# Optimization experiments

Measured on AMD Instinct MI355X. Metric: run time of the kernel, lower is better.

Reference implementation:

```python
import jax, jax.numpy as jnp
import numpy as np

N, M, E, H = 4096, 16384, 512, 8
D = E // H  # head dim = 64


def _rms(x, g, eps=1e-6):
    return x * jax.lax.rsqrt(jnp.mean(jnp.square(x), axis=-1, keepdims=True) + eps) * g


def _split(x):
    # (rows, E) -> (rows, H, D)
    return x.reshape(x.shape[0], H, D)


def _sdpa(q, k, v):
    # Faithful to the source layout: SDPA on (rows, H, D) tensors, i.e. per-row
    # attention over the H heads (tiny HxH softmax per node).
    s = jnp.einsum('nhd,ngd->nhg', q, k) / jnp.sqrt(jnp.asarray(D, q.dtype))
    a = jax.nn.softmax(s, axis=-1)
    return jnp.einsum('nhg,ngd->nhd', a, v).reshape(-1, E)


def setup_inputs() -> dict:
    key = jax.random.key(0)
    ks = jax.random.split(key, 25)
    w = lambda k, s, sc: jax.random.normal(k, s, dtype=jnp.float32) * sc
    se = 1.0 / np.sqrt(E)   # Linear(E, E) init scale
    sm = 1.0 / np.sqrt(M)   # Linear(M, N) init scale
    inp = {
        'x_node': jax.random.normal(ks[0], (N, E), dtype=jnp.float32),
        'x_edge': jax.random.normal(ks[1], (M, E), dtype=jnp.float32),
        # sparse-ish binary adjacency, avg degree ~8
        'adj': (jax.random.uniform(ks[2], (N, N)) < 0.002).astype(jnp.float32),
        # per-branch QKV weights (4 separate MultiHeadAttention modules)
        'Wq_hh': w(ks[3], (E, E), se), 'Wk_hh': w(ks[4], (E, E), se), 'Wv_hh': w(ks[5], (E, E), se),
        'Wq_ee': w(ks[6], (E, E), se), 'Wk_ee': w(ks[7], (E, E), se), 'Wv_ee': w(ks[8], (E, E), se),
        'Wq_he': w(ks[9], (E, E), se), 'Wk_he': w(ks[10], (E, E), se), 'Wv_he': w(ks[11], (E, E), se),
        'Wq_eh': w(ks[12], (E, E), se), 'Wk_eh': w(ks[13], (E, E), se), 'Wv_eh': w(ks[14], (E, E), se),
        # shape_proj (edges -> nodes) weights, one per module that uses it
        'Wp1_he': w(ks[15], (N, M), sm),
        'Wp1_eh': w(ks[16], (N, M), sm),
        'Wp1_ee': w(ks[17], (N, M), sm),
        # RMSNorm gains
        'g_n': jnp.ones((E,), jnp.float32),
        'g_e': jnp.ones((E,), jnp.float32),
        'g2': jnp.ones((E,), jnp.float32),
        # FeedForward
        'Wf1': w(ks[18], (E, 4 * E), se), 'bf1': jnp.zeros((4 * E,), jnp.float32),
        'Wf2': w(ks[19], (4 * E, E), 1.0 / np.sqrt(4 * E)), 'bf2': jnp.zeros((E,), jnp.float32),
    }
    return inp


def reference(x_node, x_edge, adj,
              Wq_hh, Wk_hh, Wv_hh, Wq_ee, Wk_ee, Wv_ee,
              Wq_he, Wk_he, Wv_he, Wq_eh, Wk_eh, Wv_eh,
              Wp1_he, Wp1_eh, Wp1_ee,
              g_n, g_e, g2, Wf1, bf1, Wf2, bf2):
    h = _rms(x_node, g_n)   # (N, E)
    e = _rms(x_edge, g_e)   # (M, E)

    # hh: adjacency injected into the node query branch
    q = jnp.einsum('nm,mhd->nhd', adj, _split(h @ Wq_hh))
    out_hh = _sdpa(q, _split(h @ Wk_hh), _split(h @ Wv_hh))

    # ee: edge queries/keys projected to node rows via shape_proj
    q = jnp.einsum('nm,mhd->nhd', Wp1_ee, _split(e @ Wq_ee))
    k = jnp.einsum('nm,mhd->nhd', Wp1_ee, _split(e @ Wk_ee))
    out_ee = _sdpa(q, k, _split(h @ Wv_ee))

    # eh: edge query projected to node rows, node key
    q = jnp.einsum('nm,mhd->nhd', Wp1_eh, _split(e @ Wq_eh))
    out_eh = _sdpa(q, _split(h @ Wk_eh), _split(h @ Wv_eh))

    # he: node query, edge key projected to node rows
    k = jnp.einsum('nm,mhd->nhd', Wp1_he, _split(e @ Wk_he))
    out_he = _sdpa(_split(h @ Wq_he), k, _split(h @ Wv_he))

    x = out_hh + out_ee + out_eh + out_he          # (N, E)
    y = _rms(x, g2)
    return jax.nn.gelu(y @ Wf1 + bf1, approximate=False) @ Wf2 + bf2
```

## Files before the change

kernel.cpp:

```cpp
#include <hip/hip_runtime.h>
#include <cstdint>


typedef unsigned short u16;
typedef __bf16 bf16x8 __attribute__((ext_vector_type(8)));
typedef float f32x4 __attribute__((ext_vector_type(4)));

__device__ __forceinline__ u16 f2bf(float f) {
    unsigned u = __float_as_uint(f);
    return (u16)((u + 0x7fffu + ((u >> 16) & 1u)) >> 16);
}
__device__ __forceinline__ float bf2f(u16 u) { return __uint_as_float(((unsigned)u) << 16); }
__device__ __forceinline__ float gelu_exact(float x) {
    return 0.5f * x * (1.0f + erff(x * 0.70710678118654752f));
}

__device__ __forceinline__ void gload_lds16(const void* g, void* l) {
    __builtin_amdgcn_global_load_lds(
        (const __attribute__((address_space(1))) unsigned int*)(uintptr_t)g,
        (__attribute__((address_space(3))) unsigned int*)(unsigned int)(uintptr_t)l,
        16, 0, 0);
}

#define SCHED0 __builtin_amdgcn_sched_barrier(0)

__device__ __forceinline__ void swz_block(int& bx, int& by, int& bz) {
    const int nx = gridDim.x, ny = gridDim.y;
    const int nwg = nx * ny * gridDim.z;
    int lin = blockIdx.x + nx * (blockIdx.y + ny * blockIdx.z);
    const int chunk = nwg >> 3;
    lin = (lin & 7) * chunk + (lin >> 3);
    bx = lin % nx;
    lin /= nx;
    by = lin % ny;
    bz = lin / ny;
}

template <bool SWZ>
__global__ __launch_bounds__(256) void cvt_f32_bf16(const float* __restrict__ in,
                                                    u16* __restrict__ out, size_t n8) {
    size_t i = (size_t)blockIdx.x * 256 + threadIdx.x;
    size_t stride = (size_t)gridDim.x * 256;
    for (; i < n8; i += stride) {
        float4 a = ((const float4*)in)[i * 2];
        float4 b = ((const float4*)in)[i * 2 + 1];
        u16 r[8] = {f2bf(a.x), f2bf(a.y), f2bf(a.z), f2bf(a.w),
                    f2bf(b.x), f2bf(b.y), f2bf(b.z), f2bf(b.w)};
        size_t o = i;
        if constexpr (SWZ) o = (i & ~(size_t)63) | ((i & 63) ^ ((i >> 7) & 3));
        ((uint4*)out)[o] = *(const uint4*)r;
    }
}

__global__ __launch_bounds__(256) void transpose_cvt(const float* __restrict__ in,
                                                     u16* __restrict__ out, int R, int C) {
    __shared__ float tile[32][33];
    int c0 = blockIdx.x * 32, r0 = blockIdx.y * 32;
    int tx = threadIdx.x & 31, ty = threadIdx.x >> 5;
#pragma unroll
    for (int i = 0; i < 4; ++i)
        tile[ty + i * 8][tx] = in[(size_t)(r0 + ty + i * 8) * C + c0 + tx];
    __syncthreads();
#pragma unroll
    for (int i = 0; i < 4; ++i) {
        int orow = c0 + ty + i * 8;
        out[(size_t)orow * R + ((r0 + tx) ^ (((orow >> 1) & 3) << 3))] = f2bf(tile[tx][ty + i * 8]);
    }
}

struct W12 { const float* in[12]; u16* out[12]; };
__global__ __launch_bounds__(256) void transpose_cvt12(W12 w) {
    __shared__ float tile[32][33];
    const float* in = w.in[blockIdx.z];
    u16* out = w.out[blockIdx.z];
    int c0 = blockIdx.x * 32, r0 = blockIdx.y * 32;
    int tx = threadIdx.x & 31, ty = threadIdx.x >> 5;
#pragma unroll
    for (int i = 0; i < 4; ++i)
        tile[ty + i * 8][tx] = in[(size_t)(r0 + ty + i * 8) * 512 + c0 + tx];
    __syncthreads();
#pragma unroll
    for (int i = 0; i < 4; ++i) {
        int orow = c0 + ty + i * 8;
        out[(size_t)orow * 512 + ((r0 + tx) ^ (((orow >> 1) & 3) << 3))] = f2bf(tile[tx][ty + i * 8]);
    }
}

__global__ __launch_bounds__(256) void transpose_u16(const u16* __restrict__ in,
                                                     u16* __restrict__ out, int R, int C) {
    __shared__ u16 tile[32][34];
    int c0 = blockIdx.x * 32, r0 = blockIdx.y * 32;
    int tx = threadIdx.x & 31, ty = threadIdx.x >> 5;
#pragma unroll
    for (int i = 0; i < 4; ++i)
        tile[ty + i * 8][tx] = in[(size_t)(r0 + ty + i * 8) * C + c0 + tx];
    __syncthreads();
#pragma unroll
    for (int i = 0; i < 4; ++i) {
        int orow = c0 + ty + i * 8;
        out[(size_t)orow * R + ((r0 + tx) ^ (((orow >> 1) & 3) << 3))] = tile[tx][ty + i * 8];
    }
}

template <bool SWZ>
__global__ __launch_bounds__(256) void rmsnorm_bf16(const float* __restrict__ x,
                                                    const float* __restrict__ g,
                                                    u16* __restrict__ out) {
    int row = blockIdx.x, tid = threadIdx.x;
    const float* xr = x + (size_t)row * 512;
    float2 v = *(const float2*)(xr + tid * 2);
    float ss = v.x * v.x + v.y * v.y;
#pragma unroll
    for (int o = 32; o; o >>= 1) ss += __shfl_down(ss, o);
    __shared__ float red[4];
    if ((tid & 63) == 0) red[tid >> 6] = ss;
    __syncthreads();
    float tot = red[0] + red[1] + red[2] + red[3];
    float rs = rsqrtf(tot * (1.0f / 512.0f) + 1e-6f);
    unsigned pack = (unsigned)f2bf(v.x * rs * g[tid * 2]) |
                    ((unsigned)f2bf(v.y * rs * g[tid * 2 + 1]) << 16);
    int o32 = SWZ ? (tid ^ (((row >> 1) & 3) << 2)) : tid;
    ((unsigned*)out)[(size_t)row * 256 + o32] = pack;
}

__global__ __launch_bounds__(256) void adj_spmm(const float* __restrict__ adj,
                                                const u16* __restrict__ h,
                                                u16* __restrict__ out) {
    const int wave = threadIdx.x >> 6, lane = threadIdx.x & 63;
    const int n = blockIdx.x * 4 + wave;
    const float* arow = adj + (size_t)n * 4096;
    float acc[8] = {0.f, 0.f, 0.f, 0.f, 0.f, 0.f, 0.f, 0.f};
    for (int j = 0; j < 64; ++j) {
        float v = arow[j * 64 + lane];
        unsigned long long mask = __ballot(v != 0.0f);
        while (mask) {
            int bit = __ffsll((long long)mask) - 1;
            mask &= mask - 1;
            int m = j * 64 + bit;
            float w = __shfl(v, bit);
            int cs = (lane & ~3) | ((lane & 3) ^ ((m >> 1) & 3));
            uint4 q = *(const uint4*)(h + (size_t)m * 512 + cs * 8);
            const u16* qu = (const u16*)&q;
#pragma unroll
            for (int t = 0; t < 8; ++t) acc[t] += w * bf2f(qu[t]);
        }
    }
    int co = (lane & ~3) | ((lane & 3) ^ ((n >> 1) & 3));
    u16 r[8];
#pragma unroll
    for (int t = 0; t < 8; ++t) r[t] = f2bf(acc[t]);
    *(uint4*)(out + (size_t)n * 512 + co * 8) = *(const uint4*)r;
}

template <int MODE>
__device__ __forceinline__ void gemm_tile_body(const u16* __restrict__ A,
                                               const u16* __restrict__ Bt,
                                               int N, int K, int k_begin, int k_end,
                                               int rowStart, int colStart,
                                               void* __restrict__ C,
                                               const float* __restrict__ bias) {
    __shared__ u16 Asm[128 * 32];
    __shared__ u16 Bsm[128 * 32];
    const int tid = threadIdx.x;
    const int wave = tid >> 6, lane = tid & 63;
    const int wr = wave >> 1, wc = wave & 1;

    f32x4 acc[4][4];
#pragma unroll
    for (int m = 0; m < 4; ++m)
#pragma unroll
        for (int n = 0; n < 4; ++n) acc[m][n] = f32x4{0.f, 0.f, 0.f, 0.f};

    const int off0 = (wave * 2 + 0) * 1024 + lane * 16;
    const int off1 = (wave * 2 + 1) * 1024 + lane * 16;
    const int r0 = off0 >> 6, k0e = (off0 & 63) >> 1;
    const int r1 = off1 >> 6, k1e = (off1 & 63) >> 1;
    const size_t Arow0 = (size_t)(rowStart + r0) * K + k0e;
    const size_t Arow1 = (size_t)(rowStart + r1) * K + k1e;
    const size_t Brow0 = (size_t)(colStart + r0) * K + k0e;
    const size_t Brow1 = (size_t)(colStart + r1) * K + k1e;
    u16* As0 = &Asm[(wave * 2 + 0) * 512];
    u16* As1 = &Asm[(wave * 2 + 1) * 512];
    u16* Bs0 = &Bsm[(wave * 2 + 0) * 512];
    u16* Bs1 = &Bsm[(wave * 2 + 1) * 512];

    const int rsel = lane & 15, ksel = lane >> 4;
    const int fsw = (ksel ^ ((rsel >> 1) & 3)) << 3;

    for (int kk = k_begin; kk < k_end; kk += 32) {
        gload_lds16(A + Arow0 + kk, As0);
        gload_lds16(A + Arow1 + kk, As1);
        gload_lds16(Bt + Brow0 + kk, Bs0);
        gload_lds16(Bt + Brow1 + kk, Bs1);
        __syncthreads();
        bf16x8 aF[4], bF[4];
#pragma unroll
        for (int m = 0; m < 4; ++m)
            aF[m] = *(const bf16x8*)&Asm[(wr * 64 + m * 16 + rsel) * 32 + fsw];
#pragma unroll
        for (int n = 0; n < 4; ++n)
            bF[n] = *(const bf16x8*)&Bsm[(wc * 64 + n * 16 + rsel) * 32 + fsw];
#pragma unroll
        for (int m = 0; m < 4; ++m)
#pragma unroll
            for (int n = 0; n < 4; ++n)
                acc[m][n] = __builtin_amdgcn_mfma_f32_16x16x32_bf16(aF[m], bF[n], acc[m][n], 0, 0, 0);
        __syncthreads();
    }

    const int cq = (lane >> 4) * 4, cr = lane & 15;
#pragma unroll
    for (int m = 0; m < 4; ++m) {
#pragma unroll
        for (int n = 0; n < 4; ++n) {
            int col = colStart + wc * 64 + n * 16 + cr;
#pragma unroll
            for (int j = 0; j < 4; ++j) {
                int row = rowStart + wr * 64 + m * 16 + cq + j;
                float v = acc[m][n][j];
                if constexpr (MODE == 0) {
                    ((u16*)C)[(size_t)row * N + col] = f2bf(v);
                } else if constexpr (MODE == 1) {
                    v = gelu_exact(v + bias[col]);
                    ((u16*)C)[(size_t)row * N + (col ^ (((row >> 1) & 3) << 3))] = f2bf(v);
                } else {
                    if (bias) v += bias[col];
                    atomicAdd(&((float*)C)[(size_t)row * N + col], v);
                }
            }
        }
    }
}

template <int MODE>
__global__ __launch_bounds__(256) void gemm_bt(const u16* __restrict__ A,
                                               const u16* __restrict__ Bt,
                                               void* __restrict__ C,
                                               const float* __restrict__ bias,
                                               int N, int K, int kLen) {
    int bx, by, bz;
    swz_block(bx, by, bz);
    const float* bb = (MODE == 3) ? ((bz == 0) ? bias : nullptr) : bias;
    int kb = bz * kLen;
    gemm_tile_body<MODE>(A, Bt, N, K, kb, kb + kLen, by * 128, bx * 128, C, bb);
}

struct Small12 { const u16* A[12]; const u16* W[12]; u16* C[12]; };
__global__ __launch_bounds__(256) void gemm_small12(Small12 s) {
    int bx, by, bz;
    swz_block(bx, by, bz);
    gemm_tile_body<0>(s.A[bz], s.W[bz], 512, 512, 0, 512, by * 128, bx * 128, s.C[bz], nullptr);
}

struct Big3 { const float* A[3]; };
__global__ __launch_bounds__(256, 2) void gemm_f32a(Big3 ba, const u16* __restrict__ Bt,
                                                    float* __restrict__ C0, int K) {
    __shared__ float Afs[3][4096];
    __shared__ u16 Bsm[3][4096];
    const int i = blockIdx.x;
    const int x = i & 7, j = i >> 3;
    const int bx = j & 3;
    const int g = x * 48 + (j >> 2);
    const int by = g & 31, bz = g >> 5;
    const int mat = bz >> 2, ks = bz & 3;
    const float* __restrict__ A = ba.A[mat];
    float* __restrict__ C = C0 + (size_t)mat * (4096 * 512);
    const int rowStart = by * 128, colStart = bx * 128;
    const int kLen = 4096;
    const int k0 = ks * kLen;

    const int tid = threadIdx.x;
    const int wave = tid >> 6, lane = tid & 63;
    const int wr = wave >> 1, wc = wave & 1;

    f32x4 acc[4][4];
#pragma unroll
    for (int mm = 0; mm < 4; ++mm)
#pragma unroll
        for (int n = 0; n < 4; ++n) acc[mm][n] = f32x4{0.f, 0.f, 0.f, 0.f};

    const int lrow = lane >> 3;
    const int slot = (lane & 7) ^ lrow;
    size_t asrc[4];
    int adst[4];
#pragma unroll
    for (int ii = 0; ii < 4; ++ii) {
        int row = wave * 32 + ii * 8 + lrow;
        asrc[ii] = (size_t)(rowStart + row) * K + slot * 4;
        adst[ii] = (wave * 4 + ii) * 256 + lane * 4;
    }

    const int off0 = (wave * 2 + 0) * 1024 + lane * 16;
    const int off1 = (wave * 2 + 1) * 1024 + lane * 16;
    const int br0 = off0 >> 6, bk0 = (off0 & 63) >> 1;
    const int br1 = off1 >> 6, bk1 = (off1 & 63) >> 1;
    const u16* Bp0 = Bt + (size_t)(colStart + br0) * K + bk0;
    const u16* Bp1 = Bt + (size_t)(colStart + br1) * K + bk1;
    const int ws0 = (wave * 2 + 0) * 512, ws1 = (wave * 2 + 1) * 512;

    const int rsel = lane & 15, ksel = lane >> 4;
    const int fsw = (ksel ^ ((rsel >> 1) & 3)) << 3;

    auto STAGE = [&](int buf, int kk) {
#pragma unroll
        for (int ii = 0; ii < 4; ++ii)
            gload_lds16(A + asrc[ii] + kk, &Afs[buf][adst[ii]]);
        gload_lds16(Bp0 + kk, &Bsm[buf][ws0]);
        gload_lds16(Bp1 + kk, &Bsm[buf][ws1]);
    };
    auto COMPUTE = [&](int buf) {
        bf16x8 aF[4], bF[4];
#pragma unroll
        for (int mm = 0; mm < 4; ++mm) {
            int R = wr * 64 + mm * 16 + rsel;
            const char* rb = (const char*)&Afs[buf][0] + R * 128;
            f32x4 lo = *(const f32x4*)(rb + ((((ksel << 1) | 0) ^ (R & 7)) << 4));
            f32x4 hi = *(const f32x4*)(rb + ((((ksel << 1) | 1) ^ (R & 7)) << 4));
            aF[mm][0] = (__bf16)lo[0]; aF[mm][1] = (__bf16)lo[1];
            aF[mm][2] = (__bf16)lo[2]; aF[mm][3] = (__bf16)lo[3];
            aF[mm][4] = (__bf16)hi[0]; aF[mm][5] = (__bf16)hi[1];
            aF[mm][6] = (__bf16)hi[2]; aF[mm][7] = (__bf16)hi[3];
        }
#pragma unroll
        for (int n = 0; n < 4; ++n)
            bF[n] = *(const bf16x8*)&Bsm[buf][(wc * 64 + n * 16 + rsel) * 32 + fsw];
#pragma unroll
        for (int mm = 0; mm < 4; ++mm)
#pragma unroll
            for (int n = 0; n < 4; ++n)
                acc[mm][n] = __builtin_amdgcn_mfma_f32_16x16x32_bf16(aF[mm], bF[n], acc[mm][n], 0, 0, 0);
    };
    auto STEP = [&](int sbuf, int cbuf, int kk) {
        STAGE(sbuf, kk);
        SCHED0;
        asm volatile("s_waitcnt vmcnt(12)");
        SCHED0;
        __builtin_amdgcn_s_barrier();
        SCHED0;
        COMPUTE(cbuf);
        SCHED0;
        __builtin_amdgcn_s_barrier();
        SCHED0;
    };

    STAGE(0, k0);
    STAGE(1, k0 + 32);
    SCHED0;

    int kk = k0 + 64;
    for (int it = 0; it < 42; ++it) {
        STEP(2, 0, kk);
        STEP(0, 1, kk + 32);
        STEP(1, 2, kk + 64);
        kk += 96;
    }
    asm volatile("s_waitcnt vmcnt(6)");
    SCHED0;
    __builtin_amdgcn_s_barrier();
    SCHED0;
    COMPUTE(0);
    SCHED0;
    __builtin_amdgcn_s_barrier();
    SCHED0;
    asm volatile("s_waitcnt vmcnt(0)");
    SCHED0;
    __builtin_amdgcn_s_barrier();
    SCHED0;
    COMPUTE(1);

    const int cq = (lane >> 4) * 4, cr = lane & 15;
#pragma unroll
    for (int mm = 0; mm < 4; ++mm)
#pragma unroll
        for (int n = 0; n < 4; ++n) {
            int col = colStart + wc * 64 + n * 16 + cr;
#pragma unroll
            for (int jj = 0; jj < 4; ++jj) {
                int row = rowStart + wr * 64 + mm * 16 + cq + jj;
                atomicAdd(&C[(size_t)row * 512 + col], acc[mm][n][jj]);
            }
        }
}

struct SP12 { const u16* p[12]; };
__global__ __launch_bounds__(256) void sdpa_fused(SP12 sp, const float* __restrict__ g2,
                                                  u16* __restrict__ y) {
    __shared__ float qb[4][8][65], kb[4][8][65], vb[4][8][65];
    __shared__ float aw[4][64];
    __shared__ float red[4];
    const int n = blockIdx.x, tid = threadIdx.x;
    const size_t base = (size_t)n * 512;
    const int e0 = tid * 2, hs = e0 >> 6, ds = e0 & 63;

#pragma unroll
    for (int br = 0; br < 4; ++br) {
        unsigned u;
        u = *(const unsigned*)(sp.p[br * 3 + 0] + base + e0);
        qb[br][hs][ds] = bf2f(u & 0xffffu); qb[br][hs][ds + 1] = bf2f(u >> 16);
        u = *(const unsigned*)(sp.p[br * 3 + 1] + base + e0);
        kb[br][hs][ds] = bf2f(u & 0xffffu); kb[br][hs][ds + 1] = bf2f(u >> 16);
        u = *(const unsigned*)(sp.p[br * 3 + 2] + base + e0);
        vb[br][hs][ds] = bf2f(u & 0xffffu); vb[br][hs][ds + 1] = bf2f(u >> 16);
    }
    __syncthreads();

    const int b = tid >> 6, h = (tid >> 3) & 7, g = tid & 7;
    float s = 0.f;
    const float* qr = &qb[b][h][0];
    const float* kr = &kb[b][g][0];
#pragma unroll
    for (int j = 0; j < 64; ++j) s += qr[j] * kr[j];
    s *= 0.125f;
    float mx = s;
#pragma unroll
    for (int o = 1; o < 8; o <<= 1) mx = fmaxf(mx, __shfl_xor(mx, o));
    float p = expf(s - mx);
    float sm = p;
#pragma unroll
    for (int o = 1; o < 8; o <<= 1) sm += __shfl_xor(sm, o);
    aw[b][(h << 3) | g] = p / sm;
    __syncthreads();

    float o0 = 0.f, o1 = 0.f;
#pragma unroll
    for (int bb = 0; bb < 4; ++bb)
#pragma unroll
        for (int gg = 0; gg < 8; ++gg) {
            float a = aw[bb][(hs << 3) | gg];
            o0 += a * vb[bb][gg][ds];
            o1 += a * vb[bb][gg][ds + 1];
        }

    float ss = o0 * o0 + o1 * o1;
#pragma unroll
    for (int o = 32; o; o >>= 1) ss += __shfl_down(ss, o);
    if ((tid & 63) == 0) red[tid >> 6] = ss;
    __syncthreads();
    float tot = red[0] + red[1] + red[2] + red[3];
    float rs = rsqrtf(tot * (1.0f / 512.0f) + 1e-6f);
    unsigned pack = (unsigned)f2bf(o0 * rs * g2[e0]) | ((unsigned)f2bf(o1 * rs * g2[e0 + 1]) << 16);
    ((unsigned*)y)[(size_t)n * 256 + (tid ^ (((n >> 1) & 3) << 2))] = pack;
}

extern "C" void kernel_launch(void* const* d_in, const int* in_sizes, int n_in,
                              void* d_out, int out_size, void* d_ws, size_t ws_size,
                              hipStream_t stream) {
    (void)in_sizes; (void)n_in; (void)out_size; (void)ws_size;
    const int N = 4096, M = 16384, E = 512;

    const float* x_node = (const float*)d_in[0];
    const float* x_edge = (const float*)d_in[1];
    const float* adj    = (const float*)d_in[2];
    const float* Wp1_he = (const float*)d_in[15];
    const float* Wp1_eh = (const float*)d_in[16];
    const float* Wp1_ee = (const float*)d_in[17];
    const float* g_n = (const float*)d_in[18];
    const float* g_e = (const float*)d_in[19];
    const float* g2  = (const float*)d_in[20];
    const float* Wf1 = (const float*)d_in[21];
    const float* bf1 = (const float*)d_in[22];
    const float* Wf2 = (const float*)d_in[23];
    const float* bf2 = (const float*)d_in[24];

    char* p = (char*)d_ws;
    auto alloc = [&](size_t b) { char* r = p; p += (b + 255) & ~(size_t)255; return r; };
    const size_t NP = (size_t)N * E;
    const size_t WSZ = (size_t)E * E;
    u16* h    = (u16*)alloc(NP * 2);
    u16* e    = (u16*)alloc((size_t)M * E * 2);
    u16* eT   = (u16*)alloc((size_t)M * E * 2);
    u16* Wt   = (u16*)alloc(12 * WSZ * 2);
    u16* Wf1T = (u16*)alloc((size_t)2048 * 512 * 2);
    u16* Wf2T = (u16*)alloc((size_t)512 * 2048 * 2);
    float* F3 = (float*)alloc(3 * NP * 4);
    u16* P3b  = (u16*)alloc(3 * NP * 2);
    u16* Ahb  = (u16*)alloc(NP * 2);
    u16* S12  = (u16*)alloc(12 * NP * 2);
    u16* y    = (u16*)alloc(NP * 2);
    u16* t    = (u16*)alloc((size_t)N * 2048 * 2);

    W12 w12;
    for (int i = 0; i < 12; ++i) { w12.in[i] = (const float*)d_in[3 + i]; w12.out[i] = Wt + i * WSZ; }
    transpose_cvt12<<<dim3(16, 16, 12), 256, 0, stream>>>(w12);
    transpose_cvt<<<dim3(64, 16), 256, 0, stream>>>(Wf1, Wf1T, 512, 2048);
    transpose_cvt<<<dim3(16, 64), 256, 0, stream>>>(Wf2, Wf2T, 2048, 512);

    rmsnorm_bf16<true><<<N, 256, 0, stream>>>(x_node, g_n, h);
    rmsnorm_bf16<false><<<M, 256, 0, stream>>>(x_edge, g_e, e);
    transpose_u16<<<dim3(16, 512), 256, 0, stream>>>(e, eT, M, 512);
    adj_spmm<<<1024, 256, 0, stream>>>(adj, h, Ahb);

    hipMemsetAsync(F3, 0, 3 * NP * 4, stream);
    Big3 bp; bp.A[0] = Wp1_ee; bp.A[1] = Wp1_eh; bp.A[2] = Wp1_he;
    gemm_f32a<<<dim3(1536), 256, 0, stream>>>(bp, eT, F3, M);
    cvt_f32_bf16<true><<<2048, 256, 0, stream>>>(F3, P3b, 3 * NP / 8);
    const u16* Peeb = P3b + 0 * NP;
    const u16* Pehb = P3b + 1 * NP;
    const u16* Pheb = P3b + 2 * NP;

    Small12 sb;
    const u16* aList[12] = {Ahb, h, h, Peeb, Peeb, h, Pehb, h, h, h, Pheb, h};
    const int wList[12]  = {0, 1, 2, 3, 4, 5, 9, 10, 11, 6, 7, 8};
    for (int i = 0; i < 12; ++i) {
        sb.A[i] = aList[i];
        sb.W[i] = Wt + wList[i] * WSZ;
        sb.C[i] = S12 + i * NP;
    }
    gemm_small12<<<dim3(4, 32, 12), 256, 0, stream>>>(sb);

    SP12 sp;
    for (int i = 0; i < 12; ++i) sp.p[i] = S12 + i * NP;
    sdpa_fused<<<N, 256, 0, stream>>>(sp, g2, y);

    gemm_bt<1><<<dim3(16, 32, 1), 256, 0, stream>>>(y, Wf1T, t, bf1, 2048, 512, 512);
    hipMemsetAsync(d_out, 0, NP * 4, stream);
    gemm_bt<3><<<dim3(4, 32, 2), 256, 0, stream>>>(t, Wf2T, d_out, bf2, 512, 2048, 1024);
}
```

Before: 630.4 us.

## Widen f32-A projection GEMM tile to full 512 columns with 8-way split-K

The big shape_proj GEMM (Wp1 f32 x eT bf16) now uses 512-thread blocks that each cover 128 rows by all 512 output columns, with split-K raised from 4 to 8 and the k-loop switched from triple- to double-buffered LDS. Each f32 A tile is read from global memory once instead of four times across column blocks, which cuts the dominant A traffic. In exchange there are twice as many atomicAdd partial sums into C, a larger B tile in LDS, twice the accumulator registers per wave, and a shallower prefetch pipeline that may expose load latency.

```diff
diff --git a/kernel.cpp b/kernel.cpp
--- a/kernel.cpp
+++ b/kernel.cpp
@@ -253,63 +253,63 @@
 }
 
 struct Big3 { const float* A[3]; };
-__global__ __launch_bounds__(256, 2) void gemm_f32a(Big3 ba, const u16* __restrict__ Bt,
+__global__ __launch_bounds__(512, 2) void gemm_f32a(Big3 ba, const u16* __restrict__ Bt,
                                                     float* __restrict__ C0, int K) {
-    __shared__ float Afs[3][4096];
-    __shared__ u16 Bsm[3][4096];
-    const int i = blockIdx.x;
-    const int x = i & 7, j = i >> 3;
-    const int bx = j & 3;
-    const int g = x * 48 + (j >> 2);
-    const int by = g & 31, bz = g >> 5;
-    const int mat = bz >> 2, ks = bz & 3;
+    __shared__ float Afs[2][4096];
+    __shared__ u16 Bsm[2][16384];
+    const int id = blockIdx.x;
+    const int by = id & 31, g = id >> 5;
+    const int ks = g & 7, mat = g >> 3;
     const float* __restrict__ A = ba.A[mat];
     float* __restrict__ C = C0 + (size_t)mat * (4096 * 512);
-    const int rowStart = by * 128, colStart = bx * 128;
-    const int kLen = 4096;
+    const int rowStart = by * 128;
+    const int kLen = 2048;
     const int k0 = ks * kLen;
+    const int nt = kLen >> 5;
 
     const int tid = threadIdx.x;
     const int wave = tid >> 6, lane = tid & 63;
-    const int wr = wave >> 1, wc = wave & 1;
-
-    f32x4 acc[4][4];
+    const int wr = wave >> 2, wq = wave & 3;
+
+    f32x4 acc[4][8];
 #pragma unroll
     for (int mm = 0; mm < 4; ++mm)
 #pragma unroll
-        for (int n = 0; n < 4; ++n) acc[mm][n] = f32x4{0.f, 0.f, 0.f, 0.f};
+        for (int n = 0; n < 8; ++n) acc[mm][n] = f32x4{0.f, 0.f, 0.f, 0.f};
 
     const int lrow = lane >> 3;
     const int slot = (lane & 7) ^ lrow;
-    size_t asrc[4];
-    int adst[4];
+    size_t asrc[2];
+    int adst[2];
+#pragma unroll
+    for (int ii = 0; ii < 2; ++ii) {
+        int s = wave * 2 + ii;
+        asrc[ii] = (size_t)(rowStart + s * 8 + lrow) * K + slot * 4;
+        adst[ii] = s * 256 + lane * 4;
+    }
+
+    size_t bsrc[4];
+    int bdst[4];
 #pragma unroll
     for (int ii = 0; ii < 4; ++ii) {
-        int row = wave * 32 + ii * 8 + lrow;
-        asrc[ii] = (size_t)(rowStart + row) * K + slot * 4;
-        adst[ii] = (wave * 4 + ii) * 256 + lane * 4;
-    }
-
-    const int off0 = (wave * 2 + 0) * 1024 + lane * 16;
-    const int off1 = (wave * 2 + 1) * 1024 + lane * 16;
-    const int br0 = off0 >> 6, bk0 = (off0 & 63) >> 1;
-    const int br1 = off1 >> 6, bk1 = (off1 & 63) >> 1;
-    const u16* Bp0 = Bt + (size_t)(colStart + br0) * K + bk0;
-    const u16* Bp1 = Bt + (size_t)(colStart + br1) * K + bk1;
-    const int ws0 = (wave * 2 + 0) * 512, ws1 = (wave * 2 + 1) * 512;
+        int s = wave * 4 + ii;
+        bsrc[ii] = (size_t)(s * 16 + (lane >> 2)) * K + (lane & 3) * 8;
+        bdst[ii] = s * 512 + lane * 8;
+    }
 
     const int rsel = lane & 15, ksel = lane >> 4;
     const int fsw = (ksel ^ ((rsel >> 1) & 3)) << 3;
 
     auto STAGE = [&](int buf, int kk) {
 #pragma unroll
+        for (int ii = 0; ii < 2; ++ii)
+            gload_lds16(A + asrc[ii] + kk, &Afs[buf][adst[ii]]);
+#pragma unroll
         for (int ii = 0; ii < 4; ++ii)
-            gload_lds16(A + asrc[ii] + kk, &Afs[buf][adst[ii]]);
-        gload_lds16(Bp0 + kk, &Bsm[buf][ws0]);
-        gload_lds16(Bp1 + kk, &Bsm[buf][ws1]);
+            gload_lds16(Bt + bsrc[ii] + kk, &Bsm[buf][bdst[ii]]);
     };
     auto COMPUTE = [&](int buf) {
-        bf16x8 aF[4], bF[4];
+        bf16x8 aF[4], bF[8];
 #pragma unroll
         for (int mm = 0; mm < 4; ++mm) {
             int R = wr * 64 + mm * 16 + rsel;
@@ -322,58 +322,47 @@
             aF[mm][6] = (__bf16)hi[2]; aF[mm][7] = (__bf16)hi[3];
         }
 #pragma unroll
-        for (int n = 0; n < 4; ++n)
-            bF[n] = *(const bf16x8*)&Bsm[buf][(wc * 64 + n * 16 + rsel) * 32 + fsw];
+        for (int n = 0; n < 8; ++n)
+            bF[n] = *(const bf16x8*)&Bsm[buf][(wq * 128 + n * 16 + rsel) * 32 + fsw];
 #pragma unroll
         for (int mm = 0; mm < 4; ++mm)
 #pragma unroll
-            for (int n = 0; n < 4; ++n)
+            for (int n = 0; n < 8; ++n)
                 acc[mm][n] = __builtin_amdgcn_mfma_f32_16x16x32_bf16(aF[mm], bF[n], acc[mm][n], 0, 0, 0);
     };
-    auto STEP = [&](int sbuf, int cbuf, int kk) {
-        STAGE(sbuf, kk);
-        SCHED0;
-        asm volatile("s_waitcnt vmcnt(12)");
-        SCHED0;
-        __builtin_amdgcn_s_barrier();
-        SCHED0;
-        COMPUTE(cbuf);
-        SCHED0;
-        __builtin_amdgcn_s_barrier();
-        SCHED0;
-    };
 
     STAGE(0, k0);
-    STAGE(1, k0 + 32);
-    SCHED0;
-
-    int kk = k0 + 64;
-    for (int it = 0; it < 42; ++it) {
-        STEP(2, 0, kk);
-        STEP(0, 1, kk + 32);
-        STEP(1, 2, kk + 64);
-        kk += 96;
-    }
-    asm volatile("s_waitcnt vmcnt(6)");
-    SCHED0;
-    __builtin_amdgcn_s_barrier();
-    SCHED0;
-    COMPUTE(0);
-    SCHED0;
-    __builtin_amdgcn_s_barrier();
-    SCHED0;
     asm volatile("s_waitcnt vmcnt(0)");
     SCHED0;
     __builtin_amdgcn_s_barrier();
     SCHED0;
-    COMPUTE(1);
+
+    int cur = 0;
+    for (int t = 0; t < nt - 1; ++t) {
+        STAGE(cur ^ 1, k0 + (t + 1) * 32);
+        SCHED0;
+        asm volatile("s_waitcnt vmcnt(6)");
+        SCHED0;
+        __builtin_amdgcn_s_barrier();
+        SCHED0;
+        COMPUTE(cur);
+        SCHED0;
+        __builtin_amdgcn_s_barrier();
+        SCHED0;
+        cur ^= 1;
+    }
+    asm volatile("s_waitcnt vmcnt(0)");
+    SCHED0;
+    __builtin_amdgcn_s_barrier();
+    SCHED0;
+    COMPUTE(cur);
 
     const int cq = (lane >> 4) * 4, cr = lane & 15;
 #pragma unroll
     for (int mm = 0; mm < 4; ++mm)
 #pragma unroll
-        for (int n = 0; n < 4; ++n) {
-            int col = colStart + wc * 64 + n * 16 + cr;
+        for (int n = 0; n < 8; ++n) {
+            int col = wq * 128 + n * 16 + cr;
 #pragma unroll
             for (int jj = 0; jj < 4; ++jj) {
                 int row = rowStart + wr * 64 + mm * 16 + cq + jj;
@@ -492,7 +481,7 @@
 
     hipMemsetAsync(F3, 0, 3 * NP * 4, stream);
     Big3 bp; bp.A[0] = Wp1_ee; bp.A[1] = Wp1_eh; bp.A[2] = Wp1_he;
-    gemm_f32a<<<dim3(1536), 256, 0, stream>>>(bp, eT, F3, M);
+    gemm_f32a<<<dim3(768), 512, 0, stream>>>(bp, eT, F3, M);
     cvt_f32_bf16<true><<<2048, 256, 0, stream>>>(F3, P3b, 3 * NP / 8);
     const u16* Peeb = P3b + 0 * NP;
     const u16* Pehb = P3b + 1 * NP;
```

After: 681.0 us. 8.0% more time.

## Load fp32 A operand directly to registers in shape-proj GEMM, cut LDS

Applied to the files above, without the earlier changes.

The fp32 Wp1 operand of the big edge-to-node GEMM is now read straight from global memory into registers, double-buffered in registers, and converted to bf16 there instead of being staged through LDS. Only the bf16 B tile stays in LDS, double-buffered instead of triple. Each wave now owns 32 rows by all 128 columns, and the launch uses the shared swizzle helper with occupancy raised to 3 blocks. This lowers LDS footprint and LDS read traffic, at the cost of uncoalesced-ish per-lane global loads for A and more B fragment reads per wave.

```diff
diff --git a/kernel.cpp b/kernel.cpp
--- a/kernel.cpp
+++ b/kernel.cpp
@@ -253,42 +253,30 @@
 }
 
 struct Big3 { const float* A[3]; };
-__global__ __launch_bounds__(256, 2) void gemm_f32a(Big3 ba, const u16* __restrict__ Bt,
-                                                    float* __restrict__ C0, int K) {
-    __shared__ float Afs[3][4096];
-    __shared__ u16 Bsm[3][4096];
-    const int i = blockIdx.x;
-    const int x = i & 7, j = i >> 3;
-    const int bx = j & 3;
-    const int g = x * 48 + (j >> 2);
-    const int by = g & 31, bz = g >> 5;
-    const int mat = bz >> 2, ks = bz & 3;
+__global__ __launch_bounds__(256, 3) void gemm_f32a(Big3 ba, const u16* __restrict__ Bt,
+                                                    float* __restrict__ C0, int K,
+                                                    int zPerMat, int kLen) {
+    __shared__ u16 Bsm[2][4096];
+    int bx, by, bz;
+    swz_block(bx, by, bz);
+    const int mat = bz / zPerMat, ks = bz - mat * zPerMat;
     const float* __restrict__ A = ba.A[mat];
     float* __restrict__ C = C0 + (size_t)mat * (4096 * 512);
     const int rowStart = by * 128, colStart = bx * 128;
-    const int kLen = 4096;
     const int k0 = ks * kLen;
 
     const int tid = threadIdx.x;
     const int wave = tid >> 6, lane = tid & 63;
-    const int wr = wave >> 1, wc = wave & 1;
-
-    f32x4 acc[4][4];
-#pragma unroll
-    for (int mm = 0; mm < 4; ++mm)
-#pragma unroll
-        for (int n = 0; n < 4; ++n) acc[mm][n] = f32x4{0.f, 0.f, 0.f, 0.f};
-
-    const int lrow = lane >> 3;
-    const int slot = (lane & 7) ^ lrow;
-    size_t asrc[4];
-    int adst[4];
-#pragma unroll
-    for (int ii = 0; ii < 4; ++ii) {
-        int row = wave * 32 + ii * 8 + lrow;
-        asrc[ii] = (size_t)(rowStart + row) * K + slot * 4;
-        adst[ii] = (wave * 4 + ii) * 256 + lane * 4;
-    }
+    const int rsel = lane & 15, ksel = lane >> 4;
+
+    f32x4 acc[2][8];
+#pragma unroll
+    for (int mm = 0; mm < 2; ++mm)
+#pragma unroll
+        for (int n = 0; n < 8; ++n) acc[mm][n] = f32x4{0.f, 0.f, 0.f, 0.f};
+
+    const float* Ap0 = A + (size_t)(rowStart + wave * 32 + 0 * 16 + rsel) * K + ksel * 8;
+    const float* Ap1 = A + (size_t)(rowStart + wave * 32 + 1 * 16 + rsel) * K + ksel * 8;
 
     const int off0 = (wave * 2 + 0) * 1024 + lane * 16;
     const int off1 = (wave * 2 + 1) * 1024 + lane * 16;
@@ -298,67 +286,82 @@
     const u16* Bp1 = Bt + (size_t)(colStart + br1) * K + bk1;
     const int ws0 = (wave * 2 + 0) * 512, ws1 = (wave * 2 + 1) * 512;
 
-    const int rsel = lane & 15, ksel = lane >> 4;
     const int fsw = (ksel ^ ((rsel >> 1) & 3)) << 3;
 
-    auto STAGE = [&](int buf, int kk) {
-#pragma unroll
-        for (int ii = 0; ii < 4; ++ii)
-            gload_lds16(A + asrc[ii] + kk, &Afs[buf][adst[ii]]);
+    auto STAGEB = [&](int buf, int kk) {
         gload_lds16(Bp0 + kk, &Bsm[buf][ws0]);
         gload_lds16(Bp1 + kk, &Bsm[buf][ws1]);
     };
-    auto COMPUTE = [&](int buf) {
-        bf16x8 aF[4], bF[4];
-#pragma unroll
-        for (int mm = 0; mm < 4; ++mm) {
-            int R = wr * 64 + mm * 16 + rsel;
-            const char* rb = (const char*)&Afs[buf][0] + R * 128;
-            f32x4 lo = *(const f32x4*)(rb + ((((ksel << 1) | 0) ^ (R & 7)) << 4));
-            f32x4 hi = *(const f32x4*)(rb + ((((ksel << 1) | 1) ^ (R & 7)) << 4));
-            aF[mm][0] = (__bf16)lo[0]; aF[mm][1] = (__bf16)lo[1];
-            aF[mm][2] = (__bf16)lo[2]; aF[mm][3] = (__bf16)lo[3];
-            aF[mm][4] = (__bf16)hi[0]; aF[mm][5] = (__bf16)hi[1];
-            aF[mm][6] = (__bf16)hi[2]; aF[mm][7] = (__bf16)hi[3];
-        }
-#pragma unroll
-        for (int n = 0; n < 4; ++n)
-            bF[n] = *(const bf16x8*)&Bsm[buf][(wc * 64 + n * 16 + rsel) * 32 + fsw];
-#pragma unroll
-        for (int mm = 0; mm < 4; ++mm)
-#pragma unroll
-            for (int n = 0; n < 4; ++n)
+    auto COMPUTE = [&](int buf, float4 a0, float4 a1, float4 a2, float4 a3) {
+        bf16x8 aF[2];
+        aF[0][0] = (__bf16)a0.x; aF[0][1] = (__bf16)a0.y; aF[0][2] = (__bf16)a0.z; aF[0][3] = (__bf16)a0.w;
+        aF[0][4] = (__bf16)a1.x; aF[0][5] = (__bf16)a1.y; aF[0][6] = (__bf16)a1.z; aF[0][7] = (__bf16)a1.w;
+        aF[1][0] = (__bf16)a2.x; aF[1][1] = (__bf16)a2.y; aF[1][2] = (__bf16)a2.z; aF[1][3] = (__bf16)a2.w;
+        aF[1][4] = (__bf16)a3.x; aF[1][5] = (__bf16)a3.y; aF[1][6] = (__bf16)a3.z; aF[1][7] = (__bf16)a3.w;
+        bf16x8 bF[8];
+#pragma unroll
+        for (int n = 0; n < 8; ++n)
+            bF[n] = *(const bf16x8*)&Bsm[buf][(n * 16 + rsel) * 32 + fsw];
+#pragma unroll
+        for (int mm = 0; mm < 2; ++mm)
+#pragma unroll
+            for (int n = 0; n < 8; ++n)
                 acc[mm][n] = __builtin_amdgcn_mfma_f32_16x16x32_bf16(aF[mm], bF[n], acc[mm][n], 0, 0, 0);
     };
-    auto STEP = [&](int sbuf, int cbuf, int kk) {
-        STAGE(sbuf, kk);
-        SCHED0;
-        asm volatile("s_waitcnt vmcnt(12)");
+
+    float4 e0, e1, e2, e3, o0, o1, o2, o3;
+    {
+        const float4* p0 = (const float4*)(Ap0 + k0);
+        const float4* p1 = (const float4*)(Ap1 + k0);
+        e0 = p0[0]; e1 = p0[1]; e2 = p1[0]; e3 = p1[1];
+        STAGEB(0, k0);
+    }
+    int kk = k0;
+    for (int it = 0; it < 63; ++it) {
+        {
+            const float4* p0 = (const float4*)(Ap0 + kk + 32);
+            const float4* p1 = (const float4*)(Ap1 + kk + 32);
+            o0 = p0[0]; o1 = p0[1]; o2 = p1[0]; o3 = p1[1];
+            STAGEB(1, kk + 32);
+        }
+        SCHED0;
+        asm volatile("s_waitcnt vmcnt(6)");
         SCHED0;
         __builtin_amdgcn_s_barrier();
         SCHED0;
-        COMPUTE(cbuf);
+        COMPUTE(0, e0, e1, e2, e3);
         SCHED0;
         __builtin_amdgcn_s_barrier();
         SCHED0;
-    };
-
-    STAGE(0, k0);
-    STAGE(1, k0 + 32);
-    SCHED0;
-
-    int kk = k0 + 64;
-    for (int it = 0; it < 42; ++it) {
-        STEP(2, 0, kk);
-        STEP(0, 1, kk + 32);
-        STEP(1, 2, kk + 64);
-        kk += 96;
-    }
+        {
+            const float4* p0 = (const float4*)(Ap0 + kk + 64);
+            const float4* p1 = (const float4*)(Ap1 + kk + 64);
+            e0 = p0[0]; e1 = p0[1]; e2 = p1[0]; e3 = p1[1];
+            STAGEB(0, kk + 64);
+        }
+        SCHED0;
+        asm volatile("s_waitcnt vmcnt(6)");
+        SCHED0;
+        __builtin_amdgcn_s_barrier();
+        SCHED0;
+        COMPUTE(1, o0, o1, o2, o3);
+        SCHED0;
+        __builtin_amdgcn_s_barrier();
+        SCHED0;
+        kk += 64;
+    }
+    {
+        const float4* p0 = (const float4*)(Ap0 + kk + 32);
+        const float4* p1 = (const float4*)(Ap1 + kk + 32);
+        o0 = p0[0]; o1 = p0[1]; o2 = p1[0]; o3 = p1[1];
+        STAGEB(1, kk + 32);
+    }
+    SCHED0;
     asm volatile("s_waitcnt vmcnt(6)");
     SCHED0;
     __builtin_amdgcn_s_barrier();
     SCHED0;
-    COMPUTE(0);
+    COMPUTE(0, e0, e1, e2, e3);
     SCHED0;
     __builtin_amdgcn_s_barrier();
     SCHED0;
@@ -366,17 +369,17 @@
     SCHED0;
     __builtin_amdgcn_s_barrier();
     SCHED0;
-    COMPUTE(1);
+    COMPUTE(1, o0, o1, o2, o3);
 
     const int cq = (lane >> 4) * 4, cr = lane & 15;
 #pragma unroll
-    for (int mm = 0; mm < 4; ++mm)
-#pragma unroll
-        for (int n = 0; n < 4; ++n) {
-            int col = colStart + wc * 64 + n * 16 + cr;
+    for (int mm = 0; mm < 2; ++mm)
+#pragma unroll
+        for (int n = 0; n < 8; ++n) {
+            int col = colStart + n * 16 + cr;
 #pragma unroll
             for (int jj = 0; jj < 4; ++jj) {
-                int row = rowStart + wr * 64 + mm * 16 + cq + jj;
+                int row = rowStart + wave * 32 + mm * 16 + cq + jj;
                 atomicAdd(&C[(size_t)row * 512 + col], acc[mm][n][jj]);
             }
         }
@@ -492,7 +495,7 @@
 
     hipMemsetAsync(F3, 0, 3 * NP * 4, stream);
     Big3 bp; bp.A[0] = Wp1_ee; bp.A[1] = Wp1_eh; bp.A[2] = Wp1_he;
-    gemm_f32a<<<dim3(1536), 256, 0, stream>>>(bp, eT, F3, M);
+    gemm_f32a<<<dim3(4, 32, 12), 256, 0, stream>>>(bp, eT, F3, M, 4, 4096);
     cvt_f32_bf16<true><<<2048, 256, 0, stream>>>(F3, P3b, 3 * NP / 8);
     const u16* Peeb = P3b + 0 * NP;
     const u16* Pehb = P3b + 1 * NP;
```

Result: slower. 771.1 us (+22.3%).
